# Optimization experiments

Hardware: AMD Instinct MI355X
Metric: run time of the kernel (lower is better)

Reference implementation:

```python
import jax, jax.numpy as jnp
import numpy as np
import math

BZ, SEQ, NV, VA, HA = 16, 5, 1, 8, 8
C, DSTATE, DCONV, EXPAND, NLAYER = 384, 16, 4, 2, 4
DI = EXPAND * C
DTR = math.ceil(C / 16)  # 24
NTOK = (NV + 2) * SEQ * VA * HA  # 960 multi-modal tokens
T = NTOK + 2                     # + 2 gps tokens


def _ln(x, g, b, eps=1e-5):
    m = jnp.mean(x, -1, keepdims=True)
    v = jnp.mean((x - m) ** 2, -1, keepdims=True)
    return (x - m) * jax.lax.rsqrt(v + eps) * g + b


def _mamba(x, in_w, cw, cb, xw, dtw, dtb, a_log, d, ow):
    # x: (B,T,C); Mamba with bias=False in/out proj, conv_bias=True (mamba_ssm defaults)
    xz = jnp.einsum('btc,ec->bte', x, in_w)            # (B,T,2*DI)
    xh, z = jnp.split(xz, 2, axis=-1)
    xt = jnp.swapaxes(xh, 1, 2)                        # (B,DI,T)
    xt = jax.lax.conv_general_dilated(
        xt, cw[:, None, :], (1,), [(DCONV - 1, 0)],
        feature_group_count=DI, dimension_numbers=('NCH', 'OIH', 'NCH'))
    xh = jax.nn.silu(jnp.swapaxes(xt, 1, 2) + cb)      # causal depthwise conv + SiLU
    xdbl = jnp.einsum('btd,ed->bte', xh, xw)           # (B,T,DTR+2*DS)
    dt, Bm, Cm = jnp.split(xdbl, [DTR, DTR + DSTATE], axis=-1)
    dt = jax.nn.softplus(jnp.einsum('btr,dr->btd', dt, dtw) + dtb)  # (B,T,DI)
    A = -jnp.exp(a_log)                                # (DI,DSTATE)

    def step(h, inp):
        dt_t, x_t, b_t, c_t = inp                      # (B,DI),(B,DI),(B,DS),(B,DS)
        h = h * jnp.exp(dt_t[..., None] * A) + (dt_t * x_t)[..., None] * b_t[:, None, :]
        return h, jnp.einsum('bds,bs->bd', h, c_t)

    h0 = jnp.zeros((x.shape[0], DI, DSTATE), x.dtype)
    xs = tuple(jnp.swapaxes(a, 0, 1) for a in (dt, xh, Bm, Cm))
    _, ys = jax.lax.scan(step, h0, xs)
    y = jnp.swapaxes(ys, 0, 1) + d * xh
    y = y * jax.nn.silu(z)
    return jnp.einsum('btd,cd->btc', y, ow)


def _forward(image_tensor, lidar_tensor, radar_tensor, gps, pos_emb,
             ln1_g, ln1_b, fc1_w, fc1_b, fc2_w, fc2_b,
             in_proj_w, conv_w, conv_b, x_proj_w, dt_proj_w, dt_proj_b,
             A_log, D_param, out_proj_w, ln_f_g, ln_f_b):
    bz = lidar_tensor.shape[0] // SEQ
    h, w = lidar_tensor.shape[2], lidar_tensor.shape[3]
    img = image_tensor.reshape(bz, NV * SEQ, -1, h, w)
    lid = lidar_tensor.reshape(bz, SEQ, -1, h, w)
    rad = radar_tensor.reshape(bz, SEQ, -1, h, w)
    s1, s2 = C // 3, C // 3 * 2
    cs_img = jnp.concatenate([img[:, :, :s1], lid[:, :, s1:s2], rad[:, :, s2:]], axis=2)
    cs_lid = jnp.concatenate([lid[:, :, :s1], rad[:, :, s1:s2], img[:, :, s2:]], axis=2)
    cs_rad = jnp.concatenate([rad[:, :, :s1], img[:, :, s1:s2], lid[:, :, s2:]], axis=2)
    tok = jnp.concatenate([cs_img, cs_lid, cs_rad], axis=1)     # (bz, 3*SEQ, C, h, w)
    tok = jnp.transpose(tok, (0, 1, 3, 4, 2)).reshape(bz, -1, C)
    tok = jnp.concatenate([tok, gps], axis=1)                   # (bz, T, C)
    x = pos_emb + tok                                           # dropout is identity (eval)
    for l in range(NLAYER):
        x_ln = _ln(x, ln1_g[l], ln1_b[l])
        x_fc1 = jnp.einsum('btc,ec->bte', x_ln, fc1_w[l]) + fc1_b[l]
        x_fm = _mamba(x_fc1, in_proj_w[l, 0], conv_w[l, 0], conv_b[l, 0],
                      x_proj_w[l, 0], dt_proj_w[l, 0], dt_proj_b[l, 0],
                      A_log[l, 0], D_param[l, 0], out_proj_w[l, 0])
        x_flip = jnp.flip(x_fc1, axis=1)
        x_bm = _mamba(x_flip, in_proj_w[l, 1], conv_w[l, 1], conv_b[l, 1],
                      x_proj_w[l, 1], dt_proj_w[l, 1], dt_proj_b[l, 1],
                      A_log[l, 1], D_param[l, 1], out_proj_w[l, 1])
        x_fc2 = jnp.einsum('btc,ec->bte', x_flip, fc2_w[l]) + fc2_b[l]
        x_relu = jnp.where(x_fc2 >= 0, x_fc2, 0.2 * x_fc2)      # LeakyReLU(0.2)
        x = x_bm * x_relu + x_fm * x_bm                         # note: x_bm stays flipped, as in original
    x = _ln(x, ln_f_g, ln_f_b)
    pos_out = x[:, NTOK:]
    x = x[:, :NTOK].reshape(bz, (NV + 2) * SEQ, VA, HA, C)
    x = jnp.transpose(x, (0, 1, 4, 2, 3))
    img_out = x[:, :NV * SEQ].reshape(bz * NV * SEQ, -1, h, w)
    lid_out = x[:, NV * SEQ:(NV + 1) * SEQ].reshape(bz * SEQ, -1, h, w)
    rad_out = x[:, (NV + 1) * SEQ:].reshape(bz * SEQ, -1, h, w)
    return img_out, lid_out, rad_out, pos_out


def setup_inputs() -> dict:
    key = jax.random.key(0)
    it = iter(jax.random.split(key, 24))

    def n(shape, s=0.02):
        return jax.random.normal(next(it), shape, jnp.float32) * s

    return dict(
        image_tensor=n((BZ * NV * SEQ, C, VA, HA), 1.0),
        lidar_tensor=n((BZ * SEQ, C, VA, HA), 1.0),
        radar_tensor=n((BZ * SEQ, C, VA, HA), 1.0),
        gps=n((BZ, 2, C), 1.0),
        pos_emb=n((1, T, C), 0.02),
        ln1_g=jnp.ones((NLAYER, C)), ln1_b=jnp.zeros((NLAYER, C)),
        fc1_w=n((NLAYER, C, C)), fc1_b=jnp.zeros((NLAYER, C)),
        fc2_w=n((NLAYER, C, C)), fc2_b=jnp.zeros((NLAYER, C)),
        in_proj_w=n((NLAYER, 2, 2 * DI, C)),
        conv_w=n((NLAYER, 2, DI, DCONV), 0.1),
        conv_b=jnp.zeros((NLAYER, 2, DI)),
        x_proj_w=n((NLAYER, 2, DTR + 2 * DSTATE, DI)),
        dt_proj_w=n((NLAYER, 2, DI, DTR), 0.1),
        dt_proj_b=jnp.full((NLAYER, 2, DI), -4.6, jnp.float32),  # softplus ~ 0.01
        A_log=jnp.tile(jnp.log(jnp.arange(1., DSTATE + 1, dtype=jnp.float32)), (NLAYER, 2, DI, 1)),
        D_param=jnp.ones((NLAYER, 2, DI)),
        out_proj_w=n((NLAYER, 2, C, DI)),
        ln_f_g=jnp.ones((C,)), ln_f_b=jnp.zeros((C,)),
    )


def reference(image_tensor, lidar_tensor, radar_tensor, gps, pos_emb,
              ln1_g, ln1_b, fc1_w, fc1_b, fc2_w, fc2_b,
              in_proj_w, conv_w, conv_b, x_proj_w, dt_proj_w, dt_proj_b,
              A_log, D_param, out_proj_w, ln_f_g, ln_f_b):
    return _forward(image_tensor, lidar_tensor, radar_tensor, gps, pos_emb,
                    ln1_g, ln1_b, fc1_w, fc1_b, fc2_w, fc2_b,
                    in_proj_w, conv_w, conv_b, x_proj_w, dt_proj_w, dt_proj_b,
                    A_log, D_param, out_proj_w, ln_f_g, ln_f_b)
```

## Files before the change

### kernel.cpp

```cpp
#include <hip/hip_runtime.h>
#include <cstdint>
#include <cstddef>


constexpr int BZv = 16, SEQ = 5, NV = 1;
constexpr int C = 384, DSTATE = 16, DCONV = 4, NLAYER = 4;
constexpr int DI = 768;
constexpr int DTR = 24;
constexpr int NTOK = (NV + 2) * SEQ * 64;
constexpr int T = NTOK + 2;
constexpr int M = BZv * T;
constexpr int HB = 8;
constexpr int MH = HB * T;
constexpr int XZdim = 2 * DI;
constexpr int ND = DTR + 2 * DSTATE;
constexpr int NDP = 32;
constexpr int NCHUNK = 26, TC = 37;
constexpr int NQ = 241;
constexpr size_t SEC_SZ = (size_t)BZv * SEQ * C * 64;

constexpr size_t WSZ1 = (size_t)NLAYER * C * C;
constexpr size_t WSZI = (size_t)NLAYER * 2 * 2 * DI * C;
constexpr size_t WSZO = (size_t)NLAYER * 2 * C * DI;
constexpr size_t WSZX = (size_t)NLAYER * 2 * ND * DI;
constexpr size_t WSZD = (size_t)NLAYER * 2 * DI * 32;
constexpr size_t CAST_N = 2 * WSZ1 + WSZI + WSZO + WSZX + WSZD;

typedef __attribute__((ext_vector_type(8))) short short8;
typedef __attribute__((ext_vector_type(4))) float floatx4;

#define GLOAD_LDS16(g, l)                                        \
  __builtin_amdgcn_global_load_lds(                              \
      (const __attribute__((address_space(1))) void*)(g),        \
      (__attribute__((address_space(3))) void*)(l), 16, 0, 0)

__device__ __forceinline__ void split_bf16(float v, short& hi, short& lo) {
  unsigned u = __float_as_uint(v);
  unsigned hib = u & 0xFFFF0000u;
  float r = v - __uint_as_float(hib);
  hi = (short)(hib >> 16);
  lo = (short)(__float_as_uint(r) >> 16);
}

__device__ __forceinline__ float join_bf16(short h, short l) {
  return __uint_as_float((unsigned)(unsigned short)h << 16) +
         __uint_as_float((unsigned)(unsigned short)l << 16);
}

__device__ __forceinline__ void pow16(float e1, float* e) {
  e[0] = e1;
  e[1] = e1 * e1;
  e[3] = e[1] * e[1];
  e[7] = e[3] * e[3];
  e[15] = e[7] * e[7];
  e[2] = e[1] * e[0];
  e[4] = e[3] * e[0];
  e[5] = e[3] * e[1];
  e[6] = e[5] * e[0];
  e[8] = e[7] * e[0];
  e[9] = e[7] * e[1];
  e[10] = e[9] * e[0];
  e[11] = e[7] * e[3];
  e[12] = e[11] * e[0];
  e[13] = e[11] * e[1];
  e[14] = e[13] * e[0];
}

__global__ __launch_bounds__(256) void assemble_t_k(
    const float* __restrict__ img, const float* __restrict__ lid,
    const float* __restrict__ rad, const float* __restrict__ gps,
    const float* __restrict__ pe, float* __restrict__ x) {
  __shared__ float lds[64][129];
  int blk = blockIdx.x, tid = threadIdx.x;
  if (blk < 720) {
    int b = blk / 45;
    int rem = blk % 45;
    int g_ = rem / 3, cc = rem % 3;
    int sec = g_ / 5, s = g_ % 5;
    int srow = b * 5 + s;
    int which = (cc + sec) % 3;
    const float* src = (which == 0) ? img : (which == 1 ? lid : rad);
    const float* sp = src + (size_t)srow * (C * 64) + cc * 8192;
#pragma unroll
    for (int i = 0; i < 32; i++) {
      int lin = tid + 256 * i;
      lds[lin & 63][lin >> 6] = sp[lin];
    }
    __syncthreads();
#pragma unroll
    for (int i = 0; i < 32; i++) {
      int lin = tid + 256 * i;
      int p = lin >> 7, c = lin & 127;
      int t = g_ * 64 + p;
      int ccc = cc * 128 + c;
      x[((size_t)b * T + t) * C + ccc] = lds[p][c] + pe[(size_t)t * C + ccc];
    }
  } else {
#pragma unroll
    for (int i = 0; i < 48; i++) {
      int lin = tid + 256 * i;
      int r = lin / C, c = lin % C;
      int b = r >> 1, e = r & 1;
      x[((size_t)b * T + NTOK + e) * C + c] =
          gps[((size_t)b * 2 + e) * C + c] + pe[(size_t)(NTOK + e) * C + c];
    }
  }
}

__global__ __launch_bounds__(256) void ln_fused_k(
    const float* __restrict__ x, const float* __restrict__ g,
    const float* __restrict__ b, short* __restrict__ oh,
    short* __restrict__ ol) {
  int row = blockIdx.x * 4 + (threadIdx.x >> 6);
  int lane = threadIdx.x & 63;
  const float* xr = x + (size_t)row * C;
  float v[6];
  float s = 0.f;
#pragma unroll
  for (int j = 0; j < 6; j++) {
    v[j] = xr[lane + 64 * j];
    s += v[j];
  }
#pragma unroll
  for (int o = 32; o > 0; o >>= 1) s += __shfl_xor(s, o, 64);
  float mean = s * (1.f / 384.f);
  float q = 0.f;
#pragma unroll
  for (int j = 0; j < 6; j++) {
    float d = v[j] - mean;
    q += d * d;
  }
#pragma unroll
  for (int o = 32; o > 0; o >>= 1) q += __shfl_xor(q, o, 64);
  float rstd = rsqrtf(q * (1.f / 384.f) + 1e-5f);
#pragma unroll
  for (int j = 0; j < 6; j++) {
    int c = lane + 64 * j;
    float val = (v[j] - mean) * rstd * g[c] + b[c];
    short h, l;
    split_bf16(val, h, l);
    oh[(size_t)row * C + c] = h;
    ol[(size_t)row * C + c] = l;
  }
}

__global__ __launch_bounds__(256) void ln_stats2_k(const float* __restrict__ x,
                                                   float* __restrict__ stats) {
  int row = blockIdx.x * 4 + (threadIdx.x >> 6);
  int lane = threadIdx.x & 63;
  const float* xr = x + (size_t)row * C;
  float v[6];
  float s = 0.f;
#pragma unroll
  for (int j = 0; j < 6; j++) {
    v[j] = xr[lane + 64 * j];
    s += v[j];
  }
#pragma unroll
  for (int o = 32; o > 0; o >>= 1) s += __shfl_xor(s, o, 64);
  float mean = s * (1.f / 384.f);
  float q = 0.f;
#pragma unroll
  for (int j = 0; j < 6; j++) {
    float d = v[j] - mean;
    q += d * d;
  }
#pragma unroll
  for (int o = 32; o > 0; o >>= 1) q += __shfl_xor(q, o, 64);
  if (lane == 0) {
    stats[2 * row] = mean;
    stats[2 * row + 1] = rsqrtf(q * (1.f / 384.f) + 1e-5f);
  }
}

__global__ __launch_bounds__(256) void cast_all_k(
    const float* __restrict__ fc1w, const float* __restrict__ fc2w,
    const float* __restrict__ inw, const float* __restrict__ ow,
    const float* __restrict__ xw, const float* __restrict__ dtw,
    short* __restrict__ base) {
  size_t idx = (size_t)blockIdx.x * 256 + threadIdx.x;
  const size_t o1 = WSZ1, o2 = 2 * WSZ1, o3 = o2 + WSZI, o4 = o3 + WSZO,
               o5 = o4 + WSZX;
  float v;
  short *oh, *ol;
  if (idx < o1) {
    v = fc1w[idx];
    oh = base + idx;
    ol = base + WSZ1 + idx;
  } else if (idx < o2) {
    size_t k = idx - o1;
    v = fc2w[k];
    oh = base + 2 * WSZ1 + k;
    ol = base + 3 * WSZ1 + k;
  } else if (idx < o3) {
    size_t k = idx - o2;
    v = inw[k];
    oh = base + 4 * WSZ1 + k;
    ol = base + 4 * WSZ1 + WSZI + k;
  } else if (idx < o4) {
    size_t k = idx - o3;
    v = ow[k];
    oh = base + 4 * WSZ1 + 2 * WSZI + k;
    ol = base + 4 * WSZ1 + 2 * WSZI + WSZO + k;
  } else if (idx < o5) {
    size_t k = idx - o4;
    v = xw[k];
    oh = base + 4 * WSZ1 + 2 * WSZI + 2 * WSZO + k;
    ol = base + 4 * WSZ1 + 2 * WSZI + 2 * WSZO + WSZX + k;
  } else {
    size_t k = idx - o5;
    int col = (int)(k & 31);
    size_t row = k >> 5;
    v = (col < DTR) ? dtw[row * DTR + col] : 0.f;
    oh = base + 4 * WSZ1 + 2 * WSZI + 2 * WSZO + 2 * WSZX + k;
    ol = base + 4 * WSZ1 + 2 * WSZI + 2 * WSZO + 2 * WSZX + WSZD + k;
  }
  short h, l;
  split_bf16(v, h, l);
  *oh = h;
  *ol = l;
}

template <int ACT, bool BIAS, bool FLIPA, bool OSPLIT>
__global__ __launch_bounds__(256) void mgemm_k(
    const short* __restrict__ Ah, const short* __restrict__ Al, int K,
    const short* __restrict__ Wh, const short* __restrict__ Wl, int N,
    const float* __restrict__ bias, float* __restrict__ Co, int ldc,
    short* __restrict__ Oh, short* __restrict__ Ol, int Mrows, int arow_off,
    int crow_off) {
  __shared__ __align__(16) short sAh[128 * 32];
  __shared__ __align__(16) short sAl[128 * 32];
  __shared__ __align__(16) short sBh[128 * 32];
  __shared__ __align__(16) short sBl[128 * 32];
  const int tid = threadIdx.x;
  const int wave = tid >> 6, lane = tid & 63;
  const int m0 = blockIdx.y * 128, n0 = blockIdx.x * 128;
  const int lrow = lane >> 2, lchunk = lane & 3;
  const int wm = (wave >> 1) * 64, wn = (wave & 1) * 64;
  const int frow = lane & 15, fquad = lane >> 4;

  size_t arow[2], wrow[2];
#pragma unroll
  for (int p = 0; p < 2; p++) {
    int r = p * 64 + wave * 16 + lrow;
    int lm = m0 + r;
    if (lm >= Mrows) lm = Mrows - 1;
    int g = arow_off + lm;
    if (FLIPA) {
      int bb = g / T;
      int tt = g - bb * T;
      g = bb * T + (T - 1 - tt);
    }
    arow[p] = (size_t)g * K;
    int gn = n0 + r;
    int sn = gn < N ? gn : N - 1;
    wrow[p] = (size_t)sn * K;
  }

  floatx4 acc[4][4] = {};
  for (int k0 = 0; k0 < K; k0 += 32) {
    if (k0) __syncthreads();
    const int kc = k0 + lchunk * 8;
#pragma unroll
    for (int p = 0; p < 2; p++) {
      short* lb = &sAh[(p * 64 + wave * 16) * 32];
      GLOAD_LDS16(Ah + arow[p] + kc, lb);
      lb = &sAl[(p * 64 + wave * 16) * 32];
      GLOAD_LDS16(Al + arow[p] + kc, lb);
      lb = &sBh[(p * 64 + wave * 16) * 32];
      GLOAD_LDS16(Wh + wrow[p] + kc, lb);
      lb = &sBl[(p * 64 + wave * 16) * 32];
      GLOAD_LDS16(Wl + wrow[p] + kc, lb);
    }
    __syncthreads();
    short8 ah[4], al[4], bh[4], bl[4];
#pragma unroll
    for (int i = 0; i < 4; i++) {
      int ra = (wm + i * 16 + frow) * 32 + fquad * 8;
      int rb = (wn + i * 16 + frow) * 32 + fquad * 8;
      ah[i] = *(const short8*)&sAh[ra];
      al[i] = *(const short8*)&sAl[ra];
      bh[i] = *(const short8*)&sBh[rb];
      bl[i] = *(const short8*)&sBl[rb];
    }
#pragma unroll
    for (int i = 0; i < 4; i++)
#pragma unroll
      for (int j = 0; j < 4; j++) {
        acc[i][j] = __builtin_amdgcn_mfma_f32_16x16x32_bf16(ah[i], bh[j],
                                                            acc[i][j], 0, 0, 0);
        acc[i][j] = __builtin_amdgcn_mfma_f32_16x16x32_bf16(al[i], bh[j],
                                                            acc[i][j], 0, 0, 0);
        acc[i][j] = __builtin_amdgcn_mfma_f32_16x16x32_bf16(ah[i], bl[j],
                                                            acc[i][j], 0, 0, 0);
      }
  }
#pragma unroll
  for (int i = 0; i < 4; i++) {
#pragma unroll
    for (int r = 0; r < 4; r++) {
      int gm = m0 + wm + i * 16 + fquad * 4 + r;
      if (gm >= Mrows) continue;
      int grow = crow_off + gm;
#pragma unroll
      for (int j = 0; j < 4; j++) {
        int gn = n0 + wn + j * 16 + frow;
        if (gn >= N) continue;
        float v = acc[i][j][r];
        if constexpr (BIAS) v += bias[gn];
        if constexpr (ACT == 1) v = v >= 0.f ? v : 0.2f * v;
        if constexpr (OSPLIT) {
          short h, l;
          split_bf16(v, h, l);
          Oh[(size_t)grow * N + gn] = h;
          Ol[(size_t)grow * N + gn] = l;
        } else {
          Co[(size_t)grow * ldc + gn] = v;
        }
      }
    }
  }
}

template <int ACT, bool BIAS, int OMODE>
__global__ __launch_bounds__(256) void mgemm64_k(
    const short* __restrict__ Ah, const short* __restrict__ Al, int lda, int K,
    const short* __restrict__ Wh, const short* __restrict__ Wl, int ldw, int N,
    const float* __restrict__ bias, float* __restrict__ Co, int ldc,
    short* __restrict__ Oh, short* __restrict__ Ol, int ldo,
    const float* __restrict__ e1, const float* __restrict__ e2, int Mrows,
    int crow_off) {
  __shared__ __align__(16) short sAh[64 * 32];
  __shared__ __align__(16) short sAl[64 * 32];
  __shared__ __align__(16) short sBh[64 * 32];
  __shared__ __align__(16) short sBl[64 * 32];
  const int tid = threadIdx.x;
  const int wave = tid >> 6, lane = tid & 63;
  const int m0 = blockIdx.y * 64, n0 = blockIdx.x * 64;
  const int srow = tid >> 2, schunk = tid & 3;
  const int frow = lane & 15, fquad = lane >> 4;

  int lm = m0 + srow;
  if (lm >= Mrows) lm = Mrows - 1;
  size_t aoff = (size_t)lm * lda;
  int wn_ = n0 + srow;
  if (wn_ >= N) wn_ = N - 1;
  size_t woff = (size_t)wn_ * ldw;

  floatx4 acc[4] = {};
  for (int k0 = 0; k0 < K; k0 += 32) {
    if (k0) __syncthreads();
    const int kc = k0 + schunk * 8;
    {
      short* lb = &sAh[(wave * 16) * 32];
      GLOAD_LDS16(Ah + aoff + kc, lb);
      lb = &sAl[(wave * 16) * 32];
      GLOAD_LDS16(Al + aoff + kc, lb);
      lb = &sBh[(wave * 16) * 32];
      GLOAD_LDS16(Wh + woff + kc, lb);
      lb = &sBl[(wave * 16) * 32];
      GLOAD_LDS16(Wl + woff + kc, lb);
    }
    __syncthreads();
    short8 ah[4], al[4], bh, bl;
#pragma unroll
    for (int i = 0; i < 4; i++) {
      int ra = (i * 16 + frow) * 32 + fquad * 8;
      ah[i] = *(const short8*)&sAh[ra];
      al[i] = *(const short8*)&sAl[ra];
    }
    {
      int rb = (wave * 16 + frow) * 32 + fquad * 8;
      bh = *(const short8*)&sBh[rb];
      bl = *(const short8*)&sBl[rb];
    }
#pragma unroll
    for (int i = 0; i < 4; i++) {
      acc[i] = __builtin_amdgcn_mfma_f32_16x16x32_bf16(ah[i], bh, acc[i], 0, 0, 0);
      acc[i] = __builtin_amdgcn_mfma_f32_16x16x32_bf16(al[i], bh, acc[i], 0, 0, 0);
      acc[i] = __builtin_amdgcn_mfma_f32_16x16x32_bf16(ah[i], bl, acc[i], 0, 0, 0);
    }
  }
  const int gn = n0 + wave * 16 + frow;
  if (gn < N) {
#pragma unroll
    for (int i = 0; i < 4; i++) {
#pragma unroll
      for (int r = 0; r < 4; r++) {
        int gm = m0 + i * 16 + fquad * 4 + r;
        if (gm >= Mrows) continue;
        int grow = crow_off + gm;
        float v = acc[i][r];
        if constexpr (BIAS) v += bias[gn];
        if constexpr (ACT == 2) v = (v > 20.f) ? v : __logf(1.f + __expf(v));
        if constexpr (ACT == 4) {
          size_t o = (size_t)grow * ldc + gn;
          v = e2[o] * (e1[o] + v);
        }
        if constexpr (OMODE == 1) {
          short h, l;
          split_bf16(v, h, l);
          Oh[(size_t)grow * ldo + gn] = h;
          Ol[(size_t)grow * ldo + gn] = l;
        } else if constexpr (OMODE == 2) {
          if (gn < NDP) {
            short h, l;
            split_bf16(v, h, l);
            Oh[(size_t)grow * NDP + gn] = h;
            Ol[(size_t)grow * NDP + gn] = l;
          }
          if (gn >= DTR) Co[(size_t)grow * 32 + (gn - DTR)] = v;
        } else {
          Co[(size_t)grow * ldc + gn] = v;
        }
      }
    }
  }
}

__global__ __launch_bounds__(256) void conv_k(const float* __restrict__ xz,
                                              const float* __restrict__ cw,
                                              const float* __restrict__ cb,
                                              short* __restrict__ xch,
                                              short* __restrict__ xcl) {
  int idx = blockIdx.x * 256 + threadIdx.x;
  int dh = idx % (DI / 2);
  int rem = idx / (DI / 2);
  int q = rem % NQ;
  int b = rem / NQ;
  int d = dh * 2;
  int t0 = q * 4;
  const float* base = xz + (size_t)b * T * XZdim + d;
  float4 cwa = *(const float4*)&cw[d * 4];
  float4 cwb = *(const float4*)&cw[(d + 1) * 4];
  float cb0 = cb[d], cb1 = cb[d + 1];
  float2 w[7];
#pragma unroll
  for (int j = 0; j < 7; j++) {
    int tt = t0 - 3 + j;
    w[j] = (tt >= 0 && tt < T) ? *(const float2*)(base + (size_t)tt * XZdim)
                               : make_float2(0.f, 0.f);
  }
  const float cwx[4] = {cwa.x, cwa.y, cwa.z, cwa.w};
  const float cwy[4] = {cwb.x, cwb.y, cwb.z, cwb.w};
#pragma unroll
  for (int r = 0; r < 4; r++) {
    int t = t0 + r;
    if (t >= T) break;
    float a0 = cb0, a1 = cb1;
#pragma unroll
    for (int j = 0; j < 4; j++) {
      a0 += w[r + j].x * cwx[j];
      a1 += w[r + j].y * cwy[j];
    }
    float v0 = a0 / (1.f + __expf(-a0));
    float v1 = a1 / (1.f + __expf(-a1));
    short h0, l0, h1, l1;
    split_bf16(v0, h0, l0);
    split_bf16(v1, h1, l1);
    size_t o = ((size_t)b * T + t) * DI + d;
    *(short2*)&xch[o] = make_short2(h0, h1);
    *(short2*)&xcl[o] = make_short2(l0, l1);
  }
}

__global__ __launch_bounds__(256) void scan_p1_k(
    const float* __restrict__ xzb, const short* __restrict__ xch,
    const short* __restrict__ xcl, const float* __restrict__ xdbc,
    const float* __restrict__ alog, float* __restrict__ hchk,
    float* __restrict__ sdt) {
  int d = blockIdx.x * 256 + threadIdx.x;
  int ch = blockIdx.y, b = blockIdx.z;
  float A[DSTATE], h[DSTATE];
  bool powA = true;
#pragma unroll
  for (int s = 0; s < DSTATE; s++) {
    A[s] = -expf(alog[d * DSTATE + s]);
    powA = powA && (fabsf(A[s] + (float)(s + 1)) <= 1e-4f * (float)(s + 1));
    h[s] = 0.f;
  }
  const int t0 = ch * TC;
  const float* xzr = xzb + ((size_t)b * T + t0) * XZdim;
  const short* xchr = xch + ((size_t)b * T + t0) * DI;
  const short* xclr = xcl + ((size_t)b * T + t0) * DI;
  const float* bcr = xdbc + ((size_t)b * T + t0) * 32;
  float sd = 0.f;
  if (powA) {
    for (int t = 0; t < TC; t++) {
      float dt = xzr[(size_t)t * XZdim + d];
      float xv = join_bf16(xchr[(size_t)t * DI + d], xclr[(size_t)t * DI + d]);
      float dx = dt * xv;
      const float* bc = bcr + (size_t)t * 32;
      sd += dt;
      float ev[DSTATE];
      pow16(__expf(-dt), ev);
#pragma unroll
      for (int s = 0; s < DSTATE; s++) h[s] = h[s] * ev[s] + dx * bc[s];
    }
  } else {
    for (int t = 0; t < TC; t++) {
      float dt = xzr[(size_t)t * XZdim + d];
      float xv = join_bf16(xchr[(size_t)t * DI + d], xclr[(size_t)t * DI + d]);
      float dx = dt * xv;
      const float* bc = bcr + (size_t)t * 32;
      sd += dt;
#pragma unroll
      for (int s = 0; s < DSTATE; s++)
        h[s] = h[s] * __expf(dt * A[s]) + dx * bc[s];
    }
  }
  size_t o = ((size_t)(b * NCHUNK + ch) * DSTATE) * DI + d;
#pragma unroll
  for (int s = 0; s < DSTATE; s++) hchk[o + (size_t)s * DI] = h[s];
  sdt[(size_t)(b * NCHUNK + ch) * DI + d] = sd;
}

__global__ __launch_bounds__(256) void scan_p2_k(float* __restrict__ hchk,
                                                 const float* __restrict__ sdt,
                                                 const float* __restrict__ alog) {
  int idx = blockIdx.x * 256 + threadIdx.x;
  int d = idx % DI;
  int rem = idx / DI;
  int s = rem % DSTATE, b = rem / DSTATE;
  float A = -expf(alog[d * DSTATE + s]);
  float hin = 0.f;
#pragma unroll
  for (int ch = 0; ch < NCHUNK; ch++) {
    size_t o = ((size_t)(b * NCHUNK + ch) * DSTATE + s) * DI + d;
    float P = __expf(A * sdt[(size_t)(b * NCHUNK + ch) * DI + d]);
    float hl = hchk[o];
    hchk[o] = hin;
    hin = P * hin + hl;
  }
}

__global__ __launch_bounds__(256) void scan_p3_k(
    const float* __restrict__ xzb, const short* __restrict__ xch,
    const short* __restrict__ xcl, const float* __restrict__ xdbc,
    const float* __restrict__ alog, const float* __restrict__ Dp,
    const float* __restrict__ hchk, short* __restrict__ yh,
    short* __restrict__ yl) {
  int d = blockIdx.x * 256 + threadIdx.x;
  int ch = blockIdx.y, b = blockIdx.z;
  float A[DSTATE], h[DSTATE];
  bool powA = true;
  size_t o = ((size_t)(b * NCHUNK + ch) * DSTATE) * DI + d;
#pragma unroll
  for (int s = 0; s < DSTATE; s++) {
    A[s] = -expf(alog[d * DSTATE + s]);
    powA = powA && (fabsf(A[s] + (float)(s + 1)) <= 1e-4f * (float)(s + 1));
    h[s] = hchk[o + (size_t)s * DI];
  }
  float Dd = Dp[d];
  const int t0 = ch * TC;
  const float* xzr = xzb + ((size_t)b * T + t0) * XZdim;
  const short* xchr = xch + ((size_t)b * T + t0) * DI;
  const short* xclr = xcl + ((size_t)b * T + t0) * DI;
  const float* bcr = xdbc + ((size_t)b * T + t0) * 32;
  if (powA) {
    for (int t = 0; t < TC; t++) {
      float dt = xzr[(size_t)t * XZdim + d];
      float xv = join_bf16(xchr[(size_t)t * DI + d], xclr[(size_t)t * DI + d]);
      float zv = xzr[(size_t)t * XZdim + DI + d];
      float dx = dt * xv;
      float accv = 0.f;
      const float* bc = bcr + (size_t)t * 32;
      float ev[DSTATE];
      pow16(__expf(-dt), ev);
#pragma unroll
      for (int s = 0; s < DSTATE; s++) {
        h[s] = h[s] * ev[s] + dx * bc[s];
        accv += h[s] * bc[DSTATE + s];
      }
      float y = accv + Dd * xv;
      float sz = zv / (1.f + __expf(-zv));
      float v = y * sz;
      short hh, ll;
      split_bf16(v, hh, ll);
      size_t oi = ((size_t)(b * T + t0 + t)) * DI + d;
      yh[oi] = hh;
      yl[oi] = ll;
    }
  } else {
    for (int t = 0; t < TC; t++) {
      float dt = xzr[(size_t)t * XZdim + d];
      float xv = join_bf16(xchr[(size_t)t * DI + d], xclr[(size_t)t * DI + d]);
      float zv = xzr[(size_t)t * XZdim + DI + d];
      float dx = dt * xv;
      float accv = 0.f;
      const float* bc = bcr + (size_t)t * 32;
#pragma unroll
      for (int s = 0; s < DSTATE; s++) {
        h[s] = h[s] * __expf(dt * A[s]) + dx * bc[s];
        accv += h[s] * bc[DSTATE + s];
      }
      float y = accv + Dd * xv;
      float sz = zv / (1.f + __expf(-zv));
      float v = y * sz;
      short hh, ll;
      split_bf16(v, hh, ll);
      size_t oi = ((size_t)(b * T + t0 + t)) * DI + d;
      yh[oi] = hh;
      yl[oi] = ll;
    }
  }
}

__global__ __launch_bounds__(256) void ln_scatter_k(
    const float* __restrict__ x, const float* __restrict__ stats,
    const float* __restrict__ g, const float* __restrict__ bb,
    float* __restrict__ out) {
  __shared__ float lds[64][129];
  int blk = blockIdx.x, tid = threadIdx.x;
  if (blk < 240) {
    int b = blk / 15, g_ = blk % 15;
    int sec = g_ / 5, s = g_ % 5;
    const int rbase = b * T + g_ * 64;
    for (int cc = 0; cc < 3; cc++) {
      if (cc) __syncthreads();
#pragma unroll
      for (int i = 0; i < 32; i++) {
        int lin = tid + 256 * i;
        int p = lin >> 7, c = lin & 127;
        int row = rbase + p;
        int ccc = cc * 128 + c;
        float v = x[(size_t)row * C + ccc];
        v = (v - stats[2 * row]) * stats[2 * row + 1] * g[ccc] + bb[ccc];
        lds[p][c] = v;
      }
      __syncthreads();
      size_t obase = (size_t)sec * SEC_SZ +
                     (((size_t)(b * 5 + s) * C + cc * 128) << 6);
#pragma unroll
      for (int i = 0; i < 32; i++) {
        int lin = tid + 256 * i;
        int c = lin >> 6, p = lin & 63;
        out[obase + ((size_t)c << 6) + p] = lds[p][c];
      }
    }
  } else {
#pragma unroll
    for (int i = 0; i < 48; i++) {
      int lin = tid + 256 * i;
      int r = lin / C, c = lin % C;
      int b = r >> 1, e = r & 1;
      int row = b * T + NTOK + e;
      float v = x[(size_t)row * C + c];
      v = (v - stats[2 * row]) * stats[2 * row + 1] * g[c] + bb[c];
      out[3 * SEC_SZ + ((size_t)(b * 2 + e)) * C + c] = v;
    }
  }
}

extern "C" void kernel_launch(void* const* d_in, const int* in_sizes, int n_in,
                              void* d_out, int out_size, void* d_ws,
                              size_t ws_size, hipStream_t stream) {
  const float* image = (const float*)d_in[0];
  const float* lidar = (const float*)d_in[1];
  const float* radar = (const float*)d_in[2];
  const float* gps = (const float*)d_in[3];
  const float* pe = (const float*)d_in[4];
  const float* ln1g = (const float*)d_in[5];
  const float* ln1b = (const float*)d_in[6];
  const float* fc1w = (const float*)d_in[7];
  const float* fc1b = (const float*)d_in[8];
  const float* fc2w = (const float*)d_in[9];
  const float* fc2b_ = (const float*)d_in[10];
  const float* inw = (const float*)d_in[11];
  const float* cw = (const float*)d_in[12];
  const float* cb = (const float*)d_in[13];
  const float* xw = (const float*)d_in[14];
  const float* dtw = (const float*)d_in[15];
  const float* dtb = (const float*)d_in[16];
  const float* alog = (const float*)d_in[17];
  const float* Dp = (const float*)d_in[18];
  const float* ow = (const float*)d_in[19];
  const float* lnfg = (const float*)d_in[20];
  const float* lnfb = (const float*)d_in[21];
  float* out = (float*)d_out;

  constexpr size_t MC = (size_t)M * C;
  float* ws = (float*)d_ws;
  float* x = ws;
  float* fcb = x + MC;
  float* bmfm = fcb + MC;
  float* x1f = bmfm + MC;
  float* yf = x1f + MC;
  float* xz_h = yf + MC;
  float* xcp = xz_h + (size_t)MH * XZdim;
  float* xdp = xcp + (size_t)MH * DI;
  constexpr size_t CHK_H = (size_t)HB * NCHUNK * DSTATE * DI;
  float* hchk = xdp + (size_t)MH * 64;
  float* sdtb = hchk + CHK_H;
  float* wpl = sdtb + (size_t)HB * NCHUNK * DI;
  float* stats2 = hchk;

  short* lnh = (short*)bmfm;
  short* lnl = lnh + MC;
  float* bm = bmfm;
  short* x1h = (short*)x1f;
  short* x1l = x1h + MC;
  short* yh = (short*)yf;
  short* yl = yh + (size_t)MH * DI;
  short* xch = (short*)xcp;
  short* xcl = xch + (size_t)MH * DI;
  short* xdh = (short*)xdp;
  short* xdl = xdh + (size_t)MH * NDP;
  float* xdbc = xdp + (size_t)MH * 32;

  short* wf1h = (short*)wpl;
  short* wf1l = wf1h + WSZ1;
  short* wf2h = wf1l + WSZ1;
  short* wf2l = wf2h + WSZ1;
  short* winh = wf2l + WSZ1;
  short* winl = winh + WSZI;
  short* wowh = winl + WSZI;
  short* wowl = wowh + WSZO;
  short* wxh = wowl + WSZO;
  short* wxl = wxh + WSZX;
  short* wdth = wxl + WSZX;
  short* wdtl = wdth + WSZD;

  cast_all_k<<<(int)(CAST_N / 256), 256, 0, stream>>>(fc1w, fc2w, inw, ow, xw,
                                                      dtw, (short*)wpl);

  assemble_t_k<<<721, 256, 0, stream>>>(image, lidar, radar, gps, pe, x);

  for (int l = 0; l < NLAYER; l++) {
    ln_fused_k<<<M / 4, 256, 0, stream>>>(x, ln1g + l * C, ln1b + l * C, lnh,
                                          lnl);
    mgemm_k<0, true, false, true><<<dim3(3, 121), 256, 0, stream>>>(
        lnh, lnl, C, wf1h + (size_t)l * C * C, wf1l + (size_t)l * C * C, C,
        fc1b + l * C, nullptr, 0, x1h, x1l, M, 0, 0);
    mgemm_k<1, true, true, false><<<dim3(3, 121), 256, 0, stream>>>(
        x1h, x1l, C, wf2h + (size_t)l * C * C, wf2l + (size_t)l * C * C, C,
        fc2b_ + l * C, fcb, C, nullptr, nullptr, M, 0, 0);
    for (int di = 0; di < 2; di++) {
      const int dir = 1 - di;
      size_t wo = (size_t)(l * 2 + dir);
      for (int h = 0; h < 2; h++) {
        const int roff = h * MH;
        if (dir == 0)
          mgemm_k<0, false, false, false><<<dim3(12, 61), 256, 0, stream>>>(
              x1h, x1l, C, winh + wo * 2 * DI * C, winl + wo * 2 * DI * C,
              2 * DI, nullptr, xz_h, XZdim, nullptr, nullptr, MH, roff, 0);
        else
          mgemm_k<0, false, true, false><<<dim3(12, 61), 256, 0, stream>>>(
              x1h, x1l, C, winh + wo * 2 * DI * C, winl + wo * 2 * DI * C,
              2 * DI, nullptr, xz_h, XZdim, nullptr, nullptr, MH, roff, 0);
        conv_k<<<(HB * NQ * (DI / 2)) / 256, 256, 0, stream>>>(
            xz_h, cw + wo * DI * DCONV, cb + wo * DI, xch, xcl);
        mgemm64_k<0, false, 2><<<dim3(1, 121), 256, 0, stream>>>(
            xch, xcl, DI, DI, wxh + wo * ND * DI, wxl + wo * ND * DI, DI, ND,
            nullptr, xdbc, 0, xdh, xdl, NDP, nullptr, nullptr, MH, 0);
        mgemm64_k<2, true, 0><<<dim3(12, 121), 256, 0, stream>>>(
            xdh, xdl, NDP, 32, wdth + wo * DI * 32, wdtl + wo * DI * 32, 32,
            DI, dtb + wo * DI, xz_h, XZdim, nullptr, nullptr, 0, nullptr,
            nullptr, MH, 0);
        scan_p1_k<<<dim3(3, NCHUNK, HB), 256, 0, stream>>>(
            xz_h, xch, xcl, xdbc, alog + wo * DI * DSTATE, hchk, sdtb);
        scan_p2_k<<<(HB * DSTATE * DI) / 256, 256, 0, stream>>>(
            hchk, sdtb, alog + wo * DI * DSTATE);
        scan_p3_k<<<dim3(3, NCHUNK, HB), 256, 0, stream>>>(
            xz_h, xch, xcl, xdbc, alog + wo * DI * DSTATE, Dp + wo * DI, hchk,
            yh, yl);
        if (dir == 1)
          mgemm64_k<0, false, 0><<<dim3(6, 121), 256, 0, stream>>>(
              yh, yl, DI, DI, wowh + wo * C * DI, wowl + wo * C * DI, DI, C,
              nullptr, bm, C, nullptr, nullptr, 0, nullptr, nullptr, MH, roff);
        else
          mgemm64_k<4, false, 0><<<dim3(6, 121), 256, 0, stream>>>(
              yh, yl, DI, DI, wowh + wo * C * DI, wowl + wo * C * DI, DI, C,
              nullptr, x, C, nullptr, nullptr, 0, fcb, bm, MH, roff);
      }
    }
  }
  ln_stats2_k<<<M / 4, 256, 0, stream>>>(x, stats2);
  ln_scatter_k<<<241, 256, 0, stream>>>(x, stats2, lnfg, lnfb, out);
}
```

Measured before the change: 3.091 ms.

## Pre-swizzle weights into MFMA fragment layout and load B directly to registers

Weight casting now writes the bf16 hi/lo splits in an MFMA-fragment-ordered layout. The GEMM kernels then read B operands straight from global memory into registers instead of staging them through LDS, which halves LDS usage and the associated traffic. The out-projection moves from the 64-tile kernel to the 128-tile kernel, with its fused epilogue relocated there. The scan chunking also changes from 26x37 to 13x74. Direct global B loads give up LDS reuse across waves, so each B fragment may be fetched by more than one wave.

```diff
diff --git a/kernel.cpp b/kernel.cpp
--- a/kernel.cpp
+++ b/kernel.cpp
@@ -15,16 +15,20 @@
 constexpr int XZdim = 2 * DI;
 constexpr int ND = DTR + 2 * DSTATE;
 constexpr int NDP = 32;
-constexpr int NCHUNK = 26, TC = 37;
+constexpr int NCHUNK = 13, TC = 74;
 constexpr int NQ = 241;
 constexpr size_t SEC_SZ = (size_t)BZv * SEQ * C * 64;
 
-constexpr size_t WSZ1 = (size_t)NLAYER * C * C;
-constexpr size_t WSZI = (size_t)NLAYER * 2 * 2 * DI * C;
-constexpr size_t WSZO = (size_t)NLAYER * 2 * C * DI;
-constexpr size_t WSZX = (size_t)NLAYER * 2 * ND * DI;
-constexpr size_t WSZD = (size_t)NLAYER * 2 * DI * 32;
-constexpr size_t CAST_N = 2 * WSZ1 + WSZI + WSZO + WSZX + WSZD;
+constexpr size_t SET1 = (size_t)C * C;
+constexpr size_t SETI = (size_t)2 * DI * C;
+constexpr size_t SETO = (size_t)C * DI;
+constexpr size_t SETX = (size_t)64 * DI;
+constexpr size_t SETD = (size_t)DI * 32;
+constexpr size_t WSZ1 = 4 * SET1;
+constexpr size_t WSZI = 8 * SETI;
+constexpr size_t WSZO = 8 * SETO;
+constexpr size_t WSZX = 8 * SETX;
+constexpr size_t WSZD = 8 * SETD;
 
 typedef __attribute__((ext_vector_type(8))) short short8;
 typedef __attribute__((ext_vector_type(4))) float floatx4;
@@ -173,52 +177,28 @@
   }
 }
 
-__global__ __launch_bounds__(256) void cast_all_k(
-    const float* __restrict__ fc1w, const float* __restrict__ fc2w,
-    const float* __restrict__ inw, const float* __restrict__ ow,
-    const float* __restrict__ xw, const float* __restrict__ dtw,
-    short* __restrict__ base) {
+template <int NSRC, int KSRC, int KS>
+__global__ __launch_bounds__(256) void cast_swz_k(const float* __restrict__ src,
+                                                  short* __restrict__ oh,
+                                                  short* __restrict__ ol) {
+  constexpr int NP = (NSRC + 15) & ~15;
+  constexpr size_t SETSZ = (size_t)NP * KS * 32;
+  int set = blockIdx.y;
   size_t idx = (size_t)blockIdx.x * 256 + threadIdx.x;
-  const size_t o1 = WSZ1, o2 = 2 * WSZ1, o3 = o2 + WSZI, o4 = o3 + WSZO,
-               o5 = o4 + WSZX;
-  float v;
-  short *oh, *ol;
-  if (idx < o1) {
-    v = fc1w[idx];
-    oh = base + idx;
-    ol = base + WSZ1 + idx;
-  } else if (idx < o2) {
-    size_t k = idx - o1;
-    v = fc2w[k];
-    oh = base + 2 * WSZ1 + k;
-    ol = base + 3 * WSZ1 + k;
-  } else if (idx < o3) {
-    size_t k = idx - o2;
-    v = inw[k];
-    oh = base + 4 * WSZ1 + k;
-    ol = base + 4 * WSZ1 + WSZI + k;
-  } else if (idx < o4) {
-    size_t k = idx - o3;
-    v = ow[k];
-    oh = base + 4 * WSZ1 + 2 * WSZI + k;
-    ol = base + 4 * WSZ1 + 2 * WSZI + WSZO + k;
-  } else if (idx < o5) {
-    size_t k = idx - o4;
-    v = xw[k];
-    oh = base + 4 * WSZ1 + 2 * WSZI + 2 * WSZO + k;
-    ol = base + 4 * WSZ1 + 2 * WSZI + 2 * WSZO + WSZX + k;
-  } else {
-    size_t k = idx - o5;
-    int col = (int)(k & 31);
-    size_t row = k >> 5;
-    v = (col < DTR) ? dtw[row * DTR + col] : 0.f;
-    oh = base + 4 * WSZ1 + 2 * WSZI + 2 * WSZO + 2 * WSZX + k;
-    ol = base + 4 * WSZ1 + 2 * WSZI + 2 * WSZO + 2 * WSZX + WSZD + k;
-  }
+  int e = (int)(idx & 7);
+  int lane = (int)((idx >> 3) & 63);
+  size_t rest = idx >> 9;
+  int ks = (int)(rest % KS);
+  int nf = (int)(rest / KS);
+  int n = nf * 16 + (lane & 15);
+  int k = ks * 32 + ((lane >> 4) << 3) + e;
+  float v = 0.f;
+  if (n < NSRC && k < KSRC)
+    v = src[(size_t)set * NSRC * KSRC + (size_t)n * KSRC + k];
   short h, l;
   split_bf16(v, h, l);
-  *oh = h;
-  *ol = l;
+  oh[(size_t)set * SETSZ + idx] = h;
+  ol[(size_t)set * SETSZ + idx] = l;
 }
 
 template <int ACT, bool BIAS, bool FLIPA, bool OSPLIT>
@@ -226,20 +206,21 @@
     const short* __restrict__ Ah, const short* __restrict__ Al, int K,
     const short* __restrict__ Wh, const short* __restrict__ Wl, int N,
     const float* __restrict__ bias, float* __restrict__ Co, int ldc,
-    short* __restrict__ Oh, short* __restrict__ Ol, int Mrows, int arow_off,
-    int crow_off) {
+    short* __restrict__ Oh, short* __restrict__ Ol,
+    const float* __restrict__ e1, const float* __restrict__ e2, int Mrows,
+    int arow_off, int crow_off) {
   __shared__ __align__(16) short sAh[128 * 32];
   __shared__ __align__(16) short sAl[128 * 32];
-  __shared__ __align__(16) short sBh[128 * 32];
-  __shared__ __align__(16) short sBl[128 * 32];
   const int tid = threadIdx.x;
   const int wave = tid >> 6, lane = tid & 63;
   const int m0 = blockIdx.y * 128, n0 = blockIdx.x * 128;
   const int lrow = lane >> 2, lchunk = lane & 3;
   const int wm = (wave >> 1) * 64, wn = (wave & 1) * 64;
   const int frow = lane & 15, fquad = lane >> 4;
-
-  size_t arow[2], wrow[2];
+  const int KST = K >> 5;
+  const int nfb = (n0 + wn) >> 4;
+
+  size_t arow[2];
 #pragma unroll
   for (int p = 0; p < 2; p++) {
     int r = p * 64 + wave * 16 + lrow;
@@ -252,9 +233,6 @@
       g = bb * T + (T - 1 - tt);
     }
     arow[p] = (size_t)g * K;
-    int gn = n0 + r;
-    int sn = gn < N ? gn : N - 1;
-    wrow[p] = (size_t)sn * K;
   }
 
   floatx4 acc[4][4] = {};
@@ -263,25 +241,24 @@
     const int kc = k0 + lchunk * 8;
 #pragma unroll
     for (int p = 0; p < 2; p++) {
-      short* lb = &sAh[(p * 64 + wave * 16) * 32];
-      GLOAD_LDS16(Ah + arow[p] + kc, lb);
-      lb = &sAl[(p * 64 + wave * 16) * 32];
-      GLOAD_LDS16(Al + arow[p] + kc, lb);
-      lb = &sBh[(p * 64 + wave * 16) * 32];
-      GLOAD_LDS16(Wh + wrow[p] + kc, lb);
-      lb = &sBl[(p * 64 + wave * 16) * 32];
-      GLOAD_LDS16(Wl + wrow[p] + kc, lb);
+      GLOAD_LDS16(Ah + arow[p] + kc, &sAh[(p * 64 + wave * 16) * 32]);
+      GLOAD_LDS16(Al + arow[p] + kc, &sAl[(p * 64 + wave * 16) * 32]);
+    }
+    const int ks = k0 >> 5;
+    short8 bh[4], bl[4];
+#pragma unroll
+    for (int j = 0; j < 4; j++) {
+      size_t bo = (((size_t)(nfb + j) * KST + ks) * 64 + lane) * 8;
+      bh[j] = *(const short8*)&Wh[bo];
+      bl[j] = *(const short8*)&Wl[bo];
     }
     __syncthreads();
-    short8 ah[4], al[4], bh[4], bl[4];
+    short8 ah[4], al[4];
 #pragma unroll
     for (int i = 0; i < 4; i++) {
       int ra = (wm + i * 16 + frow) * 32 + fquad * 8;
-      int rb = (wn + i * 16 + frow) * 32 + fquad * 8;
       ah[i] = *(const short8*)&sAh[ra];
       al[i] = *(const short8*)&sAl[ra];
-      bh[i] = *(const short8*)&sBh[rb];
-      bl[i] = *(const short8*)&sBl[rb];
     }
 #pragma unroll
     for (int i = 0; i < 4; i++)
@@ -309,6 +286,10 @@
         float v = acc[i][j][r];
         if constexpr (BIAS) v += bias[gn];
         if constexpr (ACT == 1) v = v >= 0.f ? v : 0.2f * v;
+        if constexpr (ACT == 4) {
+          size_t o = (size_t)grow * ldc + gn;
+          v = e2[o] * (e1[o] + v);
+        }
         if constexpr (OSPLIT) {
           short h, l;
           split_bf16(v, h, l);
@@ -325,54 +306,43 @@
 template <int ACT, bool BIAS, int OMODE>
 __global__ __launch_bounds__(256) void mgemm64_k(
     const short* __restrict__ Ah, const short* __restrict__ Al, int lda, int K,
-    const short* __restrict__ Wh, const short* __restrict__ Wl, int ldw, int N,
+    const short* __restrict__ Wh, const short* __restrict__ Wl, int N,
     const float* __restrict__ bias, float* __restrict__ Co, int ldc,
-    short* __restrict__ Oh, short* __restrict__ Ol, int ldo,
-    const float* __restrict__ e1, const float* __restrict__ e2, int Mrows,
-    int crow_off) {
+    short* __restrict__ Oh, short* __restrict__ Ol, int Mrows, int crow_off) {
   __shared__ __align__(16) short sAh[64 * 32];
   __shared__ __align__(16) short sAl[64 * 32];
-  __shared__ __align__(16) short sBh[64 * 32];
-  __shared__ __align__(16) short sBl[64 * 32];
   const int tid = threadIdx.x;
   const int wave = tid >> 6, lane = tid & 63;
   const int m0 = blockIdx.y * 64, n0 = blockIdx.x * 64;
-  const int srow = tid >> 2, schunk = tid & 3;
+  const int schunk = tid & 3;
   const int frow = lane & 15, fquad = lane >> 4;
-
-  int lm = m0 + srow;
+  const int KST = K >> 5;
+  const int nfw = (n0 >> 4) + wave;
+
+  int lm = m0 + (tid >> 2);
   if (lm >= Mrows) lm = Mrows - 1;
   size_t aoff = (size_t)lm * lda;
-  int wn_ = n0 + srow;
-  if (wn_ >= N) wn_ = N - 1;
-  size_t woff = (size_t)wn_ * ldw;
 
   floatx4 acc[4] = {};
   for (int k0 = 0; k0 < K; k0 += 32) {
     if (k0) __syncthreads();
     const int kc = k0 + schunk * 8;
+    GLOAD_LDS16(Ah + aoff + kc, &sAh[(wave * 16) * 32]);
+    GLOAD_LDS16(Al + aoff + kc, &sAl[(wave * 16) * 32]);
+    const int ks = k0 >> 5;
+    short8 bh, bl;
     {
-      short* lb = &sAh[(wave * 16) * 32];
-      GLOAD_LDS16(Ah + aoff + kc, lb);
-      lb = &sAl[(wave * 16) * 32];
-      GLOAD_LDS16(Al + aoff + kc, lb);
-      lb = &sBh[(wave * 16) * 32];
-      GLOAD_LDS16(Wh + woff + kc, lb);
-      lb = &sBl[(wave * 16) * 32];
-      GLOAD_LDS16(Wl + woff + kc, lb);
+      size_t bo = (((size_t)nfw * KST + ks) * 64 + lane) * 8;
+      bh = *(const short8*)&Wh[bo];
+      bl = *(const short8*)&Wl[bo];
     }
     __syncthreads();
-    short8 ah[4], al[4], bh, bl;
+    short8 ah[4], al[4];
 #pragma unroll
     for (int i = 0; i < 4; i++) {
       int ra = (i * 16 + frow) * 32 + fquad * 8;
       ah[i] = *(const short8*)&sAh[ra];
       al[i] = *(const short8*)&sAl[ra];
-    }
-    {
-      int rb = (wave * 16 + frow) * 32 + fquad * 8;
-      bh = *(const short8*)&sBh[rb];
-      bl = *(const short8*)&sBl[rb];
     }
 #pragma unroll
     for (int i = 0; i < 4; i++) {
@@ -393,16 +363,7 @@
         float v = acc[i][r];
         if constexpr (BIAS) v += bias[gn];
         if constexpr (ACT == 2) v = (v > 20.f) ? v : __logf(1.f + __expf(v));
-        if constexpr (ACT == 4) {
-          size_t o = (size_t)grow * ldc + gn;
-          v = e2[o] * (e1[o] + v);
-        }
-        if constexpr (OMODE == 1) {
-          short h, l;
-          split_bf16(v, h, l);
-          Oh[(size_t)grow * ldo + gn] = h;
-          Ol[(size_t)grow * ldo + gn] = l;
-        } else if constexpr (OMODE == 2) {
+        if constexpr (OMODE == 2) {
           if (gn < NDP) {
             short h, l;
             split_bf16(v, h, l);
@@ -721,8 +682,18 @@
   short* wdth = wxl + WSZX;
   short* wdtl = wdth + WSZD;
 
-  cast_all_k<<<(int)(CAST_N / 256), 256, 0, stream>>>(fc1w, fc2w, inw, ow, xw,
-                                                      dtw, (short*)wpl);
+  cast_swz_k<C, C, 12><<<dim3((int)(SET1 / 256), 4), 256, 0, stream>>>(
+      fc1w, wf1h, wf1l);
+  cast_swz_k<C, C, 12><<<dim3((int)(SET1 / 256), 4), 256, 0, stream>>>(
+      fc2w, wf2h, wf2l);
+  cast_swz_k<2 * DI, C, 12><<<dim3((int)(SETI / 256), 8), 256, 0, stream>>>(
+      inw, winh, winl);
+  cast_swz_k<C, DI, 24><<<dim3((int)(SETO / 256), 8), 256, 0, stream>>>(
+      ow, wowh, wowl);
+  cast_swz_k<ND, DI, 24><<<dim3((int)(SETX / 256), 8), 256, 0, stream>>>(
+      xw, wxh, wxl);
+  cast_swz_k<DI, DTR, 1><<<dim3((int)(SETD / 256), 8), 256, 0, stream>>>(
+      dtw, wdth, wdtl);
 
   assemble_t_k<<<721, 256, 0, stream>>>(image, lidar, radar, gps, pe, x);
 
@@ -730,11 +701,11 @@
     ln_fused_k<<<M / 4, 256, 0, stream>>>(x, ln1g + l * C, ln1b + l * C, lnh,
                                           lnl);
     mgemm_k<0, true, false, true><<<dim3(3, 121), 256, 0, stream>>>(
-        lnh, lnl, C, wf1h + (size_t)l * C * C, wf1l + (size_t)l * C * C, C,
-        fc1b + l * C, nullptr, 0, x1h, x1l, M, 0, 0);
+        lnh, lnl, C, wf1h + l * SET1, wf1l + l * SET1, C, fc1b + l * C,
+        nullptr, 0, x1h, x1l, nullptr, nullptr, M, 0, 0);
     mgemm_k<1, true, true, false><<<dim3(3, 121), 256, 0, stream>>>(
-        x1h, x1l, C, wf2h + (size_t)l * C * C, wf2l + (size_t)l * C * C, C,
-        fc2b_ + l * C, fcb, C, nullptr, nullptr, M, 0, 0);
+        x1h, x1l, C, wf2h + l * SET1, wf2l + l * SET1, C, fc2b_ + l * C, fcb,
+        C, nullptr, nullptr, nullptr, nullptr, M, 0, 0);
     for (int di = 0; di < 2; di++) {
       const int dir = 1 - di;
       size_t wo = (size_t)(l * 2 + dir);
@@ -742,21 +713,20 @@
         const int roff = h * MH;
         if (dir == 0)
           mgemm_k<0, false, false, false><<<dim3(12, 61), 256, 0, stream>>>(
-              x1h, x1l, C, winh + wo * 2 * DI * C, winl + wo * 2 * DI * C,
-              2 * DI, nullptr, xz_h, XZdim, nullptr, nullptr, MH, roff, 0);
+              x1h, x1l, C, winh + wo * SETI, winl + wo * SETI, 2 * DI, nullptr,
+              xz_h, XZdim, nullptr, nullptr, nullptr, nullptr, MH, roff, 0);
         else
           mgemm_k<0, false, true, false><<<dim3(12, 61), 256, 0, stream>>>(
-              x1h, x1l, C, winh + wo * 2 * DI * C, winl + wo * 2 * DI * C,
-              2 * DI, nullptr, xz_h, XZdim, nullptr, nullptr, MH, roff, 0);
+              x1h, x1l, C, winh + wo * SETI, winl + wo * SETI, 2 * DI, nullptr,
+              xz_h, XZdim, nullptr, nullptr, nullptr, nullptr, MH, roff, 0);
         conv_k<<<(HB * NQ * (DI / 2)) / 256, 256, 0, stream>>>(
             xz_h, cw + wo * DI * DCONV, cb + wo * DI, xch, xcl);
         mgemm64_k<0, false, 2><<<dim3(1, 121), 256, 0, stream>>>(
-            xch, xcl, DI, DI, wxh + wo * ND * DI, wxl + wo * ND * DI, DI, ND,
-            nullptr, xdbc, 0, xdh, xdl, NDP, nullptr, nullptr, MH, 0);
+            xch, xcl, DI, DI, wxh + wo * SETX, wxl + wo * SETX, ND, nullptr,
+            xdbc, 0, xdh, xdl, MH, 0);
         mgemm64_k<2, true, 0><<<dim3(12, 121), 256, 0, stream>>>(
-            xdh, xdl, NDP, 32, wdth + wo * DI * 32, wdtl + wo * DI * 32, 32,
-            DI, dtb + wo * DI, xz_h, XZdim, nullptr, nullptr, 0, nullptr,
-            nullptr, MH, 0);
+            xdh, xdl, NDP, 32, wdth + wo * SETD, wdtl + wo * SETD, DI,
+            dtb + wo * DI, xz_h, XZdim, nullptr, nullptr, MH, 0);
         scan_p1_k<<<dim3(3, NCHUNK, HB), 256, 0, stream>>>(
             xz_h, xch, xcl, xdbc, alog + wo * DI * DSTATE, hchk, sdtb);
         scan_p2_k<<<(HB * DSTATE * DI) / 256, 256, 0, stream>>>(
@@ -765,13 +735,13 @@
             xz_h, xch, xcl, xdbc, alog + wo * DI * DSTATE, Dp + wo * DI, hchk,
             yh, yl);
         if (dir == 1)
-          mgemm64_k<0, false, 0><<<dim3(6, 121), 256, 0, stream>>>(
-              yh, yl, DI, DI, wowh + wo * C * DI, wowl + wo * C * DI, DI, C,
-              nullptr, bm, C, nullptr, nullptr, 0, nullptr, nullptr, MH, roff);
+          mgemm_k<0, false, false, false><<<dim3(3, 61), 256, 0, stream>>>(
+              yh, yl, DI, wowh + wo * SETO, wowl + wo * SETO, C, nullptr, bm,
+              C, nullptr, nullptr, nullptr, nullptr, MH, 0, roff);
         else
-          mgemm64_k<4, false, 0><<<dim3(6, 121), 256, 0, stream>>>(
-              yh, yl, DI, DI, wowh + wo * C * DI, wowl + wo * C * DI, DI, C,
-              nullptr, x, C, nullptr, nullptr, 0, fcb, bm, MH, roff);
+          mgemm_k<4, false, false, false><<<dim3(3, 61), 256, 0, stream>>>(
+              yh, yl, DI, wowh + wo * SETO, wowl + wo * SETO, C, nullptr, x, C,
+              nullptr, nullptr, fcb, bm, MH, 0, roff);
       }
     }
   }
```

Measured after the change: 3.474 ms. 12.4% more time.
